# Kernel optimization log

Measured on AMD Instinct MI355X. Metric: run time of the kernel, lower is better.

Reference implementation:

```python
import jax, jax.numpy as jnp
import numpy as np

B, S, D_IN, D_E, H = 512, 100, 300, 150, 2  # batch, patches, patch feat, embed half, heads
L = S + 1  # 101 tokens with class token
EPS = 1e-5


def setup_inputs() -> dict:
    key = jax.random.key(0)
    ks = jax.random.split(key, 12)
    r = lambda k, shp, s=0.02: (jax.random.normal(k, shp, jnp.float32) * s)
    return {
        "x": jax.random.normal(ks[0], (B, S, D_IN), jnp.float32),
        "Wp": r(ks[1], (D_IN, D_E)), "bp": jnp.zeros((D_E,), jnp.float32),
        "pos_table": r(ks[2], (L, D_E), 1.0),
        "class_embed": r(ks[3], (D_E,), 1.0),
        "Wq": r(ks[4], (H, 2 * D_E, 2 * D_E)),
        "Wk": r(ks[5], (H, 2 * D_E, 2 * D_E)),
        "Wv": r(ks[6], (H, 2 * D_E, 2 * D_E)),
        "bn1_g": jnp.ones((L,), jnp.float32), "bn1_b": jnp.zeros((L,), jnp.float32),
        "Wp1": r(ks[7], (900, 300)), "bp1": jnp.zeros((300,), jnp.float32),
        "bn2_g": jnp.ones((L,), jnp.float32), "bn2_b": jnp.zeros((L,), jnp.float32),
        "fc1_W": r(ks[8], (1200, 512)), "fc1_b": jnp.zeros((512,), jnp.float32),
        "fc2_W": r(ks[9], (512, 2)), "fc2_b": jnp.zeros((2,), jnp.float32),
    }


def _batchnorm(x, g, b):
    # torch BatchNorm1d(101) on [B, 101, F]: normalize per channel (dim 1) over (B, F), training-mode batch stats
    mean = jnp.mean(x, axis=(0, 2), keepdims=True)
    var = jnp.var(x, axis=(0, 2), keepdims=True)
    return (x - mean) * jax.lax.rsqrt(var + EPS) * g[None, :, None] + b[None, :, None]


def reference(x, Wp, bp, pos_table, class_embed, Wq, Wk, Wv, bn1_g, bn1_b,
              Wp1, bp1, bn2_g, bn2_b, fc1_W, fc1_b, fc2_W, fc2_b):
    h = jax.nn.relu(x @ Wp + bp)                                   # [B,100,150]
    cls = jnp.concatenate([jnp.broadcast_to(class_embed, (B, D_E)),
                           jnp.broadcast_to(pos_table[0], (B, D_E))], axis=-1)   # [B,300]
    tok = jnp.concatenate([h, jnp.broadcast_to(pos_table[1:], (B, S, D_E))], axis=-1)  # [B,100,300]
    z = jnp.concatenate([cls[:, None, :], tok], axis=1)            # [B,101,300]
    skip1 = jax.lax.stop_gradient(z)                               # x.clone().detach()

    # multi-head self-attention (per-head Q/K/V, no 1/sqrt(d) scaling, matching source)
    Q = jnp.einsum('bsd,hde->hbse', z, Wq)                         # [H,B,101,300]
    K = jnp.einsum('bsd,hde->hbse', z, Wk)
    V = jnp.einsum('bsd,hde->hbse', z, Wv)
    attn = jax.nn.softmax(jnp.einsum('hbse,hbte->hbst', Q, K), axis=-1)  # [H,B,101,101]
    o = jnp.einsum('hbst,hbte->hbse', attn, V)                     # [H,B,101,300]
    msa = jnp.transpose(o, (1, 2, 0, 3)).reshape(B, L, H * 2 * D_E)  # concat heads -> [B,101,600]

    y = _batchnorm(msa, bn1_g, bn1_b)
    y = jnp.concatenate([y, skip1], axis=-1)                       # [B,101,900]
    skip2 = jax.lax.stop_gradient(y)
    y = jax.nn.relu(y @ Wp1 + bp1)                                 # [B,101,300]
    y = _batchnorm(y, bn2_g, bn2_b)
    y = jnp.concatenate([y, skip2], axis=-1)                       # [B,101,1200]
    out = (y[:, 0, :] @ fc1_W + fc1_b) @ fc2_W + fc2_b             # [B,2]
    return out
```

## Files before the change

kernel.cpp:

```cpp
#include <hip/hip_runtime.h>
#include <hip/hip_fp16.h>
#include <math.h>

#define BB 512
#define SS 100
#define DE 150
#define DM 300
#define LL 101
#define NH 2

typedef _Float16 f16x8 __attribute__((ext_vector_type(8)));
typedef float f32x4 __attribute__((ext_vector_type(4)));

#define WS_CLS    0
#define WS_QK     320
#define WS_S0     960
#define WS_CPOS   964
#define WS_CVEC   1200
#define WS_COLSUM 1536
#define WS_CST0   1856
#define WS_STATS  1860
#define WS_G      2176
#define WS_P3     5248
#define WS_PART1  14336
#define WS_PART2  15360
#define WS_MSA    16384
#define WS_Y1     (WS_MSA + 512*600)
#define WS_WPF    477184
#define WS_WVF    502784
#define WS_ZB16   605184
#define WS_Q0P    769024

__global__ void kC1(const float* __restrict__ pos, const float* __restrict__ cle,
                    const float* __restrict__ Wq, const float* __restrict__ Wp1,
                    const float* __restrict__ Wp, const float* __restrict__ Wv,
                    const float* __restrict__ f1W, const float* __restrict__ f2W,
                    const float* __restrict__ f1b, const float* __restrict__ f2b,
                    float* __restrict__ ws) {
  __shared__ float cls[DM];
  int b = blockIdx.x, tid = threadIdx.x;
  if (b < 35) {
    for (int i = tid; i < DM; i += 256) cls[i] = (i < DE) ? cle[i] : pos[i - DE];
    __syncthreads();
  }
  if (b < 20) {
    int p = b >> 1, h = b & 1;
    const float* wqh = Wq + h * DM * DM;
    int d0 = p * 30;
    for (int e = tid; e < DM; e += 256) {
      float acc = 0.f;
#pragma unroll
      for (int d = 0; d < 30; ++d) acc += cls[d0 + d] * wqh[(d0 + d) * DM + e];
      ws[WS_Q0P + p * 600 + h * 300 + e] = acc;
    }
  } else if (b < 35) {
    int kb = b - 20;
    for (int n = tid; n < DM; n += 256) {
      float cs = 0.f, cv = 0.f;
      for (int k = kb * 60; k < kb * 60 + 60; ++k) {
        float w = Wp1[k * 300 + n];
        if (k < 600) cs += w; else cv += cls[k - 600] * w;
      }
      ws[WS_P3 + kb * 600 + n] = cs;
      ws[WS_P3 + kb * 600 + 300 + n] = cv;
    }
  } else if (b == 35) {
    for (int i = tid; i < DM; i += 256)
      ws[WS_CLS + i] = (i < DE) ? cle[i] : pos[i - DE];
  } else if (b < 111) {
    int wave = tid >> 6, lane = tid & 63;
    int kbase = (b - 36) * 16 + wave * 4;
#pragma unroll
    for (int j = 0; j < 4; ++j) {
      int k = kbase + j;
      const float* r = f1W + k * 512;
      float a0 = 0.f, a1 = 0.f;
      for (int m = lane; m < 512; m += 64) {
        float a = r[m];
        float2 f2 = *(const float2*)&f2W[m * 2];
        a0 += a * f2.x; a1 += a * f2.y;
      }
      for (int o = 32; o; o >>= 1) { a0 += __shfl_xor(a0, o); a1 += __shfl_xor(a1, o); }
      if (!lane) { ws[WS_G + k * 2] = a0; ws[WS_G + k * 2 + 1] = a1; }
    }
  } else if (b == 111) {
    int wave = tid >> 6, lane = tid & 63;
    if (wave < 2) {
      float acc = 0.f;
      for (int m = lane; m < 512; m += 64) acc += f1b[m] * f2W[m * 2 + wave];
      for (int o = 32; o; o >>= 1) acc += __shfl_xor(acc, o);
      if (!lane) ws[WS_CST0 + wave] = f2b[wave] + acc;
    }
  } else if (b < 137) {
    int idx = (b - 112) * 256 + tid;
    int kq = idx / 160, n = idx % 160;
    f16x8 pk;
#pragma unroll
    for (int j = 0; j < 8; ++j) {
      int k = kq * 8 + j;
      float v = (k < DM && n < DE) ? Wp[k * DE + n] : 0.f;
      pk[j] = (_Float16)v;
    }
    *(f16x8*)((char*)ws + (size_t)WS_WPF * 4 + (size_t)idx * 16) = pk;
  } else {
    int idx = (b - 137) * 256 + tid;
    int h = idx / 12800, rem = idx % 12800;
    int kq = rem / 320, n = rem % 320;
    f16x8 pk;
#pragma unroll
    for (int j = 0; j < 8; ++j) {
      int k = kq * 8 + j;
      float v = (k < DM && n < DM) ? Wv[h * DM * DM + k * DM + n] : 0.f;
      pk[j] = (_Float16)v;
    }
    *(f16x8*)((char*)ws + (size_t)WS_WVF * 4 + (size_t)idx * 16) = pk;
  }
}

__global__ void kC2(const float* __restrict__ Wk, float* __restrict__ ws) {
  __shared__ float q0s[NH * DM];
  int tid = threadIdx.x;
  for (int i = tid; i < NH * DM; i += 256) {
    float s = 0.f;
#pragma unroll
    for (int p = 0; p < 10; ++p) s += ws[WS_Q0P + p * 600 + i];
    q0s[i] = s;
  }
  __syncthreads();
  int wave = tid >> 6, lane = tid & 63;
  int idx = blockIdx.x * 4 + wave;
  int h = idx / DM, d = idx % DM;
  const float* w = Wk + h * DM * DM + d * DM;
  const float* q = q0s + h * DM;
  float acc = 0.f;
  for (int e = lane; e < DM; e += 64) acc += w[e] * q[e];
  for (int o = 32; o; o >>= 1) acc += __shfl_xor(acc, o);
  if (!lane) ws[WS_QK + idx] = acc;
}

__global__ void kC3(const float* __restrict__ pos, const float* __restrict__ bp1,
                    float* __restrict__ ws) {
  int b = blockIdx.x, tid = threadIdx.x;
  int wave = tid >> 6, lane = tid & 63;
  if (b < 50) {
    int idx = b * 4 + wave;
    int tt = idx >> 1, h = idx & 1;
    const float* pr = pos + (tt + 1) * DE;
    const float* qk = ws + WS_QK + h * DM + DE;
    float acc = 0.f;
    for (int j = lane; j < DE; j += 64) acc += pr[j] * qk[j];
    for (int o = 32; o; o >>= 1) acc += __shfl_xor(acc, o);
    if (!lane) ws[WS_CPOS + idx] = acc;
  } else if (b == 50) {
    if (wave < NH) {
      float acc = 0.f;
      for (int d = lane; d < DM; d += 64) acc += ws[WS_CLS + d] * ws[WS_QK + wave * DM + d];
      for (int o = 32; o; o >>= 1) acc += __shfl_xor(acc, o);
      if (!lane) ws[WS_S0 + wave] = acc;
    }
  } else {
    for (int n = tid; n < DM; n += 256) {
      float cs = 0.f, cv = bp1[n];
      for (int p = 0; p < 15; ++p) {
        cs += ws[WS_P3 + p * 600 + n];
        cv += ws[WS_P3 + p * 600 + 300 + n];
      }
      ws[WS_COLSUM + n] = cs;
      ws[WS_CVEC + n] = cv;
    }
  }
}

__launch_bounds__(512, 4)
__global__ void kA(const float* __restrict__ x, const float* __restrict__ bp,
                   const float* __restrict__ pos, float* __restrict__ ws) {
  __shared__ __align__(16) char smem[41600];
  __half (*hb)[DE + 2] = (__half(*)[DE + 2])smem;
  _Float16* wpt0 = (_Float16*)(smem);
  _Float16* xs0  = (_Float16*)(smem + 10240);
  _Float16* wpt1 = (_Float16*)(smem + 18240);
  _Float16* xs1  = (_Float16*)(smem + 28480);
  float* aux = (float*)(smem + 36480);

  int b = blockIdx.x, tid = threadIdx.x;
  int w = tid >> 6, lane = tid & 63;
  int l16 = lane & 15, lg = lane >> 4;
  int wm = w >> 2, wn = w & 3;
  int nnt = (wn < 3) ? 3 : 1;
  int nt0 = (wn < 3) ? wn * 3 : 9;

  const float* xb = x + b * (SS * DM);
  const char* wpf = (const char*)ws + (size_t)WS_WPF * 4;
  int rowl[4];
#pragma unroll
  for (int mt = 0; mt < 4; ++mt) {
    int r = wm * 64 + mt * 16 + l16;
    rowl[mt] = (r < SS) ? r : (SS - 1);
  }

  f32x4 acc[4][3];
#pragma unroll
  for (int mt = 0; mt < 4; ++mt)
#pragma unroll
    for (int nti = 0; nti < 3; ++nti) acc[mt][nti] = (f32x4){0.f, 0.f, 0.f, 0.f};

  float xr[4][2];
  float4 wa, wb2;

#define XLOAD(S)                                                               \
  { int kc_ = (S) * 32;                                                        \
    _Pragma("unroll")                                                          \
    for (int i_ = 0; i_ < 4; ++i_) {                                           \
      int t_ = tid + 512 * i_;                                                 \
      if (t_ < 1600) {                                                         \
        int r_ = t_ >> 4, c_ = t_ & 15, k_ = kc_ + 2 * c_;                     \
        if (k_ + 1 < DM) {                                                     \
          float2 v_ = *(const float2*)(xb + r_ * DM + k_);                     \
          xr[i_][0] = v_.x; xr[i_][1] = v_.y;                                  \
        } else {                                                               \
          xr[i_][0] = (k_ < DM) ? xb[r_ * DM + k_] : 0.f;                      \
          xr[i_][1] = 0.f;                                                     \
        } } } }

#define XWRITE(XP)                                                             \
  { _Pragma("unroll")                                                          \
    for (int i_ = 0; i_ < 4; ++i_) {                                           \
      int t_ = tid + 512 * i_;                                                 \
      if (t_ < 1600) {                                                         \
        int r_ = t_ >> 4, c_ = t_ & 15;                                        \
        *(__half2*)((char*)(XP) + r_ * 80 + c_ * 4) =                          \
            __floats2half2_rn(xr[i_][0], xr[i_][1]);                           \
      } } }

#define WLOAD(S)                                                               \
  { const char* s_ = wpf + (size_t)(S) * 10240;                                \
    wa = *(const float4*)(s_ + tid * 16);                                      \
    if (tid < 128) wb2 = *(const float4*)(s_ + (tid + 512) * 16); }

#define WWRITE(WP)                                                             \
  { *(float4*)((char*)(WP) + tid * 16) = wa;                                   \
    if (tid < 128) *(float4*)((char*)(WP) + (tid + 512) * 16) = wb2; }

  XLOAD(0); WLOAD(0);
  XWRITE(xs0); WWRITE(wpt0);
  __syncthreads();

  for (int s = 0; s < 10; ++s) {
    _Float16* wc = (s & 1) ? wpt1 : wpt0;
    _Float16* xc = (s & 1) ? xs1 : xs0;
    _Float16* wnx = (s & 1) ? wpt0 : wpt1;
    _Float16* xnx = (s & 1) ? xs0 : xs1;
    if (s < 9) { WLOAD(s + 1); XLOAD(s + 1); }
    f16x8 Bf[3];
#pragma unroll
    for (int nti = 0; nti < 3; ++nti)
      if (nti < nnt)
        Bf[nti] = *(const f16x8*)(wc + ((lg * 160 + (nt0 + nti) * 16 + l16) * 8));
#pragma unroll
    for (int mt = 0; mt < 4; ++mt) {
      f16x8 Af = *(const f16x8*)(xc + rowl[mt] * 40 + lg * 8);
#pragma unroll
      for (int nti = 0; nti < 3; ++nti)
        if (nti < nnt)
          acc[mt][nti] = __builtin_amdgcn_mfma_f32_16x16x32_f16(Af, Bf[nti], acc[mt][nti], 0, 0, 0);
    }
    if (s < 9) { WWRITE(wnx); XWRITE(xnx); }
    __syncthreads();
  }

#pragma unroll
  for (int nti = 0; nti < 3; ++nti) {
    if (nti < nnt) {
      int col = (nt0 + nti) * 16 + l16;
      float bpv = (col < DE) ? bp[col] : 0.f;
#pragma unroll
      for (int mt = 0; mt < 4; ++mt) {
        int rbase = wm * 64 + mt * 16 + lg * 4;
        f32x4 v = acc[mt][nti];
#pragma unroll
        for (int reg = 0; reg < 4; ++reg) {
          int row = rbase + reg;
          if (row < SS && col < DE) {
            float hv = v[reg] + bpv;
            hb[row][col] = __float2half(hv > 0.f ? hv : 0.f);
          }
        }
      }
    }
  }
  for (int i = tid; i < DM; i += 512) {
    aux[i] = ws[WS_QK + (i / DE) * DM + (i % DE)];
    aux[DM + i] = ws[WS_CLS + i];
  }
  __syncthreads();

  if (tid < NH * SS) {
    int hh = tid / SS, tt = tid % SS;
    const __half2* hr = (const __half2*)&hb[tt][0];
    const float* qr = &aux[hh * DE];
    float s = 0.f;
    for (int j2 = 0; j2 < DE / 2; ++j2) {
      float2 hv = __half22float2(hr[j2]);
      float2 qv = *(const float2*)&qr[2 * j2];
      s += hv.x * qv.x + hv.y * qv.y;
    }
    aux[600 + hh * LL + tt + 1] = s + ws[WS_CPOS + tt * NH + hh];
  } else if (tid < NH * SS + NH) {
    int hh = tid - NH * SS;
    aux[600 + hh * LL] = ws[WS_S0 + hh];
  }
  __syncthreads();

  if (w < NH) {
    float v0 = aux[600 + w * LL + lane];
    float v1 = (lane + 64 < LL) ? aux[600 + w * LL + lane + 64] : -1e30f;
    float m = fmaxf(v0, v1);
    for (int o = 32; o; o >>= 1) m = fmaxf(m, __shfl_xor(m, o));
    float e0 = expf(v0 - m);
    float e1 = (lane + 64 < LL) ? expf(v1 - m) : 0.f;
    float s = e0 + e1;
    for (int o = 32; o; o >>= 1) s += __shfl_xor(s, o);
    float inv = 1.f / s;
    aux[802 + w * LL + lane] = e0 * inv;
    if (lane + 64 < LL) aux[802 + w * LL + lane + 64] = e1 * inv;
  }
  __syncthreads();

  __half* zb16 = (__half*)((char*)ws + (size_t)WS_ZB16 * 4);
  for (int o = tid; o < NH * DM; o += 512) {
    int hh = o / DM, d = o % DM;
    const float* p = &aux[802 + hh * LL];
    float acc2 = p[0] * aux[DM + d];
    if (d < DE) {
      for (int t = 1; t <= SS; ++t) acc2 += p[t] * __half2float(hb[t - 1][d]);
    } else {
      int dd = d - DE;
      for (int t = 1; t <= SS; ++t) acc2 += p[t] * pos[t * DE + dd];
    }
    zb16[((size_t)hh * 512 + b) * 320 + d] = __float2half(acc2);
  }
  if (tid < 40) {
    int hh = tid / 20, dd = 300 + tid % 20;
    zb16[((size_t)hh * 512 + b) * 320 + dd] = __float2half(0.f);
  }
}

__launch_bounds__(512, 4)
__global__ void kV(float* __restrict__ ws) {
  __shared__ float shp[2][8];
  int blk = blockIdx.x;
  int mtile = blk >> 2, nb = (blk >> 1) & 1, h = blk & 1;
  int tid = threadIdx.x;
  int w = tid >> 6, lane = tid & 63;
  int l16 = lane & 15, lg = lane >> 4;
  int wm = w >> 2, wn = w & 3;
  int nnt = (wn < 3) ? 3 : 1;
  int nt0 = (wn < 3) ? wn * 3 : 9;
  int mbase = mtile * 128;

  const __half* zb16 = (const __half*)((const char*)ws + (size_t)WS_ZB16 * 4) + (size_t)h * 512 * 320;
  const __half* wvf  = (const __half*)((const char*)ws + (size_t)WS_WVF * 4) + (size_t)h * 40 * 320 * 8;

  int brow[4];
#pragma unroll
  for (int mt = 0; mt < 4; ++mt) brow[mt] = mbase + wm * 64 + mt * 16 + l16;

  f32x4 acc[4][3];
#pragma unroll
  for (int mt = 0; mt < 4; ++mt)
#pragma unroll
    for (int nti = 0; nti < 3; ++nti) acc[mt][nti] = (f32x4){0.f, 0.f, 0.f, 0.f};

  for (int s = 0; s < 10; ++s) {
    f16x8 Bf[3];
#pragma unroll
    for (int nti = 0; nti < 3; ++nti)
      if (nti < nnt) {
        int n = nb * 160 + (nt0 + nti) * 16 + l16;
        Bf[nti] = *(const f16x8*)&wvf[((size_t)(s * 4 + lg) * 320 + n) * 8];
      }
#pragma unroll
    for (int mt = 0; mt < 4; ++mt) {
      f16x8 Af = *(const f16x8*)&zb16[(size_t)brow[mt] * 320 + s * 32 + lg * 8];
#pragma unroll
      for (int nti = 0; nti < 3; ++nti)
        if (nti < nnt)
          acc[mt][nti] = __builtin_amdgcn_mfma_f32_16x16x32_f16(Af, Bf[nti], acc[mt][nti], 0, 0, 0);
    }
  }

  float s_ = 0.f, ss_ = 0.f;
#pragma unroll
  for (int nti = 0; nti < 3; ++nti) {
    if (nti < nnt) {
      int col = nb * 160 + (nt0 + nti) * 16 + l16;
      if (col < DM) {
#pragma unroll
        for (int mt = 0; mt < 4; ++mt) {
          int rbase = mbase + wm * 64 + mt * 16 + lg * 4;
          f32x4 v = acc[mt][nti];
#pragma unroll
          for (int reg = 0; reg < 4; ++reg) {
            int row = rbase + reg;
            float val = v[reg];
            ws[WS_MSA + row * 600 + h * DM + col] = val;
            s_ += val; ss_ += val * val;
          }
        }
      }
    }
  }
  for (int o = 32; o; o >>= 1) { s_ += __shfl_xor(s_, o); ss_ += __shfl_xor(ss_, o); }
  if (!lane) { shp[0][w] = s_; shp[1][w] = ss_; }
  __syncthreads();
  if (!tid) {
    float S = 0.f, SS2 = 0.f;
    for (int i = 0; i < 8; ++i) { S += shp[0][i]; SS2 += shp[1][i]; }
    ws[WS_PART1 + blk * 2] = S;
    ws[WS_PART1 + blk * 2 + 1] = SS2;
  }
}

__launch_bounds__(512)
__global__ void k5(const float* __restrict__ Wp1, const float* __restrict__ g1,
                   const float* __restrict__ b1, float* __restrict__ ws) {
  __shared__ float ab[2][600];
  __shared__ float part[2][2][300];
  __shared__ float sh[2][8];
  __shared__ float s_a1, s_b1;
  int b0 = blockIdx.x * 2, tid = threadIdx.x;
  int wv = tid >> 6, ln = tid & 63;
  for (int i = tid; i < 1200; i += 512) ab[i / 600][i % 600] = ws[WS_MSA + b0 * 600 + i];
  {
    float s = 0.f, ss = 0.f;
    if (tid < 16) { s = ws[WS_PART1 + tid * 2]; ss = ws[WS_PART1 + tid * 2 + 1]; }
    for (int o = 32; o; o >>= 1) { s += __shfl_xor(s, o); ss += __shfl_xor(ss, o); }
    if (!ln) { sh[0][wv] = s; sh[1][wv] = ss; }
  }
  __syncthreads();
  if (!tid) {
    float S = 0.f, SS2 = 0.f;
    for (int i = 0; i < 8; ++i) { S += sh[0][i]; SS2 += sh[1][i]; }
    float n = (float)(BB * 600);
    float mean = S / n, var = SS2 / n - mean * mean;
    float a = (1.f / sqrtf(var + 1e-5f)) * g1[0];
    s_a1 = a; s_b1 = b1[0] - a * mean;
    if (blockIdx.x == 0) { ws[WS_STATS + 0] = a; ws[WS_STATS + 1] = s_b1; }
  }
  __syncthreads();
  int g = tid >> 8, t = tid & 255;
  int kbeg = g * 300, kend = kbeg + 300;
  for (int n = t; n < 300; n += 256) {
    float a0 = 0.f, a1v = 0.f;
    for (int k = kbeg; k < kend; ++k) {
      float wq = Wp1[k * 300 + n];
      a0 += ab[0][k] * wq;
      a1v += ab[1][k] * wq;
    }
    part[g][0][n] = a0;
    part[g][1][n] = a1v;
  }
  __syncthreads();
  float a1 = s_a1, beta1 = s_b1;
  float s2 = 0.f, ss2 = 0.f;
  for (int n = tid; n < 300; n += 512) {
    float c = beta1 * ws[WS_COLSUM + n] + ws[WS_CVEC + n];
    float v0 = a1 * (part[0][0][n] + part[1][0][n]) + c;
    float v1 = a1 * (part[0][1][n] + part[1][1][n]) + c;
    v0 = v0 > 0.f ? v0 : 0.f;
    v1 = v1 > 0.f ? v1 : 0.f;
    ws[WS_Y1 + b0 * 300 + n] = v0;
    ws[WS_Y1 + (b0 + 1) * 300 + n] = v1;
    s2 += v0 + v1; ss2 += v0 * v0 + v1 * v1;
  }
  for (int o = 32; o; o >>= 1) { s2 += __shfl_xor(s2, o); ss2 += __shfl_xor(ss2, o); }
  if (!ln) { sh[0][wv] = s2; sh[1][wv] = ss2; }
  __syncthreads();
  if (!tid) {
    float S = 0.f, SS2 = 0.f;
    for (int i = 0; i < 8; ++i) { S += sh[0][i]; SS2 += sh[1][i]; }
    ws[WS_PART2 + blockIdx.x * 2] = S;
    ws[WS_PART2 + blockIdx.x * 2 + 1] = SS2;
  }
}

__launch_bounds__(256)
__global__ void k7(const float* __restrict__ g2, const float* __restrict__ b2,
                   float* __restrict__ out, const float* __restrict__ ws) {
  __shared__ float Gs[2400];
  __shared__ float sh[2][4];
  __shared__ float cc[4];
  int tid = threadIdx.x, wv = tid >> 6, ln = tid & 63;
  for (int i = tid; i < 2400; i += 256) Gs[i] = ws[WS_G + i];
  {
    float s = ws[WS_PART2 + tid * 2], ss = ws[WS_PART2 + tid * 2 + 1];
    for (int o = 32; o; o >>= 1) { s += __shfl_xor(s, o); ss += __shfl_xor(ss, o); }
    if (!ln) { sh[0][wv] = s; sh[1][wv] = ss; }
  }
  __syncthreads();
  if (!tid) {
    float S = 0.f, SS2 = 0.f;
    for (int i = 0; i < 4; ++i) { S += sh[0][i]; SS2 += sh[1][i]; }
    float n = (float)(BB * 300);
    float mean = S / n, var = SS2 / n - mean * mean;
    float a = (1.f / sqrtf(var + 1e-5f)) * g2[0];
    cc[0] = a; cc[1] = b2[0] - a * mean;
  }
  __syncthreads();
  if (tid < 2) {
    int c = tid;
    float sg1 = 0.f, sg2 = 0.f, sg3 = 0.f;
    for (int k = 0; k < 300; ++k) sg1 += Gs[k * 2 + c];
    for (int k = 300; k < 900; ++k) sg2 += Gs[k * 2 + c];
    for (int j = 0; j < 300; ++j) sg3 += ws[WS_CLS + j] * Gs[(900 + j) * 2 + c];
    cc[2 + c] = ws[WS_CST0 + c] + sg3 + cc[1] * sg1 + ws[WS_STATS + 1] * sg2;
  }
  __syncthreads();
  int b = blockIdx.x * 4 + wv;
  float a1 = ws[WS_STATS + 0], a2 = cc[0];
  const float* y1 = ws + WS_Y1 + b * 300;
  const float* ms = ws + WS_MSA + b * 600;
  float o0 = 0.f, o1 = 0.f, p0 = 0.f, p1 = 0.f;
  for (int k = ln; k < 300; k += 64) { float v = y1[k]; o0 += v * Gs[k * 2]; o1 += v * Gs[k * 2 + 1]; }
  for (int j = ln; j < 600; j += 64) { float v = ms[j]; p0 += v * Gs[(300 + j) * 2]; p1 += v * Gs[(300 + j) * 2 + 1]; }
  for (int o = 32; o; o >>= 1) {
    o0 += __shfl_xor(o0, o); o1 += __shfl_xor(o1, o);
    p0 += __shfl_xor(p0, o); p1 += __shfl_xor(p1, o);
  }
  if (!ln) {
    out[b * 2] = a2 * o0 + a1 * p0 + cc[2];
    out[b * 2 + 1] = a2 * o1 + a1 * p1 + cc[3];
  }
}

extern "C" void kernel_launch(void* const* d_in, const int* in_sizes, int n_in,
                              void* d_out, int out_size, void* d_ws, size_t ws_size,
                              hipStream_t stream) {
  const float* x    = (const float*)d_in[0];
  const float* Wp   = (const float*)d_in[1];
  const float* bp   = (const float*)d_in[2];
  const float* pos  = (const float*)d_in[3];
  const float* cle  = (const float*)d_in[4];
  const float* Wq   = (const float*)d_in[5];
  const float* Wk   = (const float*)d_in[6];
  const float* Wv   = (const float*)d_in[7];
  const float* bn1g = (const float*)d_in[8];
  const float* bn1b = (const float*)d_in[9];
  const float* Wp1  = (const float*)d_in[10];
  const float* bp1  = (const float*)d_in[11];
  const float* bn2g = (const float*)d_in[12];
  const float* bn2b = (const float*)d_in[13];
  const float* f1W  = (const float*)d_in[14];
  const float* f1b  = (const float*)d_in[15];
  const float* f2W  = (const float*)d_in[16];
  const float* f2b  = (const float*)d_in[17];
  float* ws = (float*)d_ws;
  float* out = (float*)d_out;

  hipLaunchKernelGGL(kC1, dim3(237), dim3(256), 0, stream, pos, cle, Wq, Wp1, Wp, Wv, f1W, f2W, f1b, f2b, ws);
  hipLaunchKernelGGL(kC2, dim3(150), dim3(256), 0, stream, Wk, ws);
  hipLaunchKernelGGL(kC3, dim3(52), dim3(256), 0, stream, pos, bp1, ws);
  hipLaunchKernelGGL(kA, dim3(512), dim3(512), 0, stream, x, bp, pos, ws);
  hipLaunchKernelGGL(kV, dim3(16), dim3(512), 0, stream, ws);
  hipLaunchKernelGGL(k5, dim3(256), dim3(512), 0, stream, Wp1, bn1g, bn1b, ws);
  hipLaunchKernelGGL(k7, dim3(128), dim3(256), 0, stream, bn2g, bn2b, out, ws);
}
```

Baseline: 117.1 us.

## Convert k5 projection GEMM to fp16 MFMA using packed MSA and Wp1 tiles

kV now also writes an fp16 copy of the MSA output, padded to 608 columns. kC1 gains extra blocks that pack the first 600 rows of Wp1 into fp16 k-octets. k5 changes from a scalar FP32 two-rows-per-block loop (256 blocks) to an MFMA 16x16x32 tiled GEMM over 128-row by 160-column tiles (8 blocks), with the BN-affine, ReLU and partial-stats epilogue fused in. The aim is to replace slow scalar FMA work on the 512x600x300 product with matrix cores, at the cost of fp16 precision loss and only 8 blocks of parallelism.

```diff
diff --git a/kernel.cpp b/kernel.cpp
--- a/kernel.cpp
+++ b/kernel.cpp
@@ -30,6 +30,8 @@
 #define WS_WVF    502784
 #define WS_ZB16   605184
 #define WS_Q0P    769024
+#define WS_MSA16  775040
+#define WS_WP1F   930688
 
 __global__ void kC1(const float* __restrict__ pos, const float* __restrict__ cle,
                     const float* __restrict__ Wq, const float* __restrict__ Wp1,
@@ -102,7 +104,7 @@
       pk[j] = (_Float16)v;
     }
     *(f16x8*)((char*)ws + (size_t)WS_WPF * 4 + (size_t)idx * 16) = pk;
-  } else {
+  } else if (b < 237) {
     int idx = (b - 137) * 256 + tid;
     int h = idx / 12800, rem = idx % 12800;
     int kq = rem / 320, n = rem % 320;
@@ -114,6 +116,17 @@
       pk[j] = (_Float16)v;
     }
     *(f16x8*)((char*)ws + (size_t)WS_WVF * 4 + (size_t)idx * 16) = pk;
+  } else {
+    int idx = (b - 237) * 256 + tid;
+    int kq = idx / 320, n = idx % 320;
+    f16x8 pk;
+#pragma unroll
+    for (int j = 0; j < 8; ++j) {
+      int k = kq * 8 + j;
+      float v = (k < 600 && n < DM) ? Wp1[k * 300 + n] : 0.f;
+      pk[j] = (_Float16)v;
+    }
+    *(f16x8*)((char*)ws + (size_t)WS_WP1F * 4 + (size_t)idx * 16) = pk;
   }
 }
 
@@ -360,6 +373,7 @@
 
   const __half* zb16 = (const __half*)((const char*)ws + (size_t)WS_ZB16 * 4) + (size_t)h * 512 * 320;
   const __half* wvf  = (const __half*)((const char*)ws + (size_t)WS_WVF * 4) + (size_t)h * 40 * 320 * 8;
+  __half* msa16h = (__half*)((char*)ws + (size_t)WS_MSA16 * 4);
 
   int brow[4];
 #pragma unroll
@@ -404,10 +418,17 @@
             int row = rbase + reg;
             float val = v[reg];
             ws[WS_MSA + row * 600 + h * DM + col] = val;
+            msa16h[(size_t)row * 608 + h * DM + col] = __float2half(val);
             s_ += val; ss_ += val * val;
           }
         }
       }
+    }
+  }
+  if (nb == 1 && h == 1) {
+    for (int i = tid; i < 128 * 8; i += 512) {
+      int r = mbase + (i >> 3), c = 600 + (i & 7);
+      msa16h[(size_t)r * 608 + c] = __float2half(0.f);
     }
   }
   for (int o = 32; o; o >>= 1) { s_ += __shfl_xor(s_, o); ss_ += __shfl_xor(ss_, o); }
@@ -421,21 +442,29 @@
   }
 }
 
-__launch_bounds__(512)
-__global__ void k5(const float* __restrict__ Wp1, const float* __restrict__ g1,
-                   const float* __restrict__ b1, float* __restrict__ ws) {
-  __shared__ float ab[2][600];
-  __shared__ float part[2][2][300];
+__launch_bounds__(512, 4)
+__global__ void k5(const float* __restrict__ g1, const float* __restrict__ b1,
+                   float* __restrict__ ws) {
   __shared__ float sh[2][8];
-  __shared__ float s_a1, s_b1;
-  int b0 = blockIdx.x * 2, tid = threadIdx.x;
-  int wv = tid >> 6, ln = tid & 63;
-  for (int i = tid; i < 1200; i += 512) ab[i / 600][i % 600] = ws[WS_MSA + b0 * 600 + i];
+  __shared__ float s_ab[2];
+  int blk = blockIdx.x;
+  int mtile = blk >> 1, nb = blk & 1;
+  int tid = threadIdx.x;
+  int w = tid >> 6, lane = tid & 63;
+  int l16 = lane & 15, lg = lane >> 4;
+  int wm = w >> 2, wn = w & 3;
+  int nnt = (wn < 3) ? 3 : 1;
+  int nt0 = (wn < 3) ? wn * 3 : 9;
+  int mbase = mtile * 128;
+
+  const __half* msa16h = (const __half*)((const char*)ws + (size_t)WS_MSA16 * 4);
+  const __half* wp1f   = (const __half*)((const char*)ws + (size_t)WS_WP1F * 4);
+
   {
     float s = 0.f, ss = 0.f;
     if (tid < 16) { s = ws[WS_PART1 + tid * 2]; ss = ws[WS_PART1 + tid * 2 + 1]; }
     for (int o = 32; o; o >>= 1) { s += __shfl_xor(s, o); ss += __shfl_xor(ss, o); }
-    if (!ln) { sh[0][wv] = s; sh[1][wv] = ss; }
+    if (!lane) { sh[0][w] = s; sh[1][w] = ss; }
   }
   __syncthreads();
   if (!tid) {
@@ -444,43 +473,71 @@
     float n = (float)(BB * 600);
     float mean = S / n, var = SS2 / n - mean * mean;
     float a = (1.f / sqrtf(var + 1e-5f)) * g1[0];
-    s_a1 = a; s_b1 = b1[0] - a * mean;
-    if (blockIdx.x == 0) { ws[WS_STATS + 0] = a; ws[WS_STATS + 1] = s_b1; }
-  }
-  __syncthreads();
-  int g = tid >> 8, t = tid & 255;
-  int kbeg = g * 300, kend = kbeg + 300;
-  for (int n = t; n < 300; n += 256) {
-    float a0 = 0.f, a1v = 0.f;
-    for (int k = kbeg; k < kend; ++k) {
-      float wq = Wp1[k * 300 + n];
-      a0 += ab[0][k] * wq;
-      a1v += ab[1][k] * wq;
-    }
-    part[g][0][n] = a0;
-    part[g][1][n] = a1v;
-  }
-  __syncthreads();
-  float a1 = s_a1, beta1 = s_b1;
+    s_ab[0] = a; s_ab[1] = b1[0] - a * mean;
+    if (blk == 0) { ws[WS_STATS + 0] = a; ws[WS_STATS + 1] = s_ab[1]; }
+  }
+  __syncthreads();
+
+  int brow[4];
+#pragma unroll
+  for (int mt = 0; mt < 4; ++mt) brow[mt] = mbase + wm * 64 + mt * 16 + l16;
+
+  f32x4 acc[4][3];
+#pragma unroll
+  for (int mt = 0; mt < 4; ++mt)
+#pragma unroll
+    for (int nti = 0; nti < 3; ++nti) acc[mt][nti] = (f32x4){0.f, 0.f, 0.f, 0.f};
+
+  for (int s = 0; s < 19; ++s) {
+    f16x8 Bf[3];
+#pragma unroll
+    for (int nti = 0; nti < 3; ++nti)
+      if (nti < nnt) {
+        int n = nb * 160 + (nt0 + nti) * 16 + l16;
+        Bf[nti] = *(const f16x8*)&wp1f[((size_t)(s * 4 + lg) * 320 + n) * 8];
+      }
+#pragma unroll
+    for (int mt = 0; mt < 4; ++mt) {
+      f16x8 Af = *(const f16x8*)&msa16h[(size_t)brow[mt] * 608 + s * 32 + lg * 8];
+#pragma unroll
+      for (int nti = 0; nti < 3; ++nti)
+        if (nti < nnt)
+          acc[mt][nti] = __builtin_amdgcn_mfma_f32_16x16x32_f16(Af, Bf[nti], acc[mt][nti], 0, 0, 0);
+    }
+  }
+
+  float a1 = s_ab[0], beta1 = s_ab[1];
   float s2 = 0.f, ss2 = 0.f;
-  for (int n = tid; n < 300; n += 512) {
-    float c = beta1 * ws[WS_COLSUM + n] + ws[WS_CVEC + n];
-    float v0 = a1 * (part[0][0][n] + part[1][0][n]) + c;
-    float v1 = a1 * (part[0][1][n] + part[1][1][n]) + c;
-    v0 = v0 > 0.f ? v0 : 0.f;
-    v1 = v1 > 0.f ? v1 : 0.f;
-    ws[WS_Y1 + b0 * 300 + n] = v0;
-    ws[WS_Y1 + (b0 + 1) * 300 + n] = v1;
-    s2 += v0 + v1; ss2 += v0 * v0 + v1 * v1;
+#pragma unroll
+  for (int nti = 0; nti < 3; ++nti) {
+    if (nti < nnt) {
+      int col = nb * 160 + (nt0 + nti) * 16 + l16;
+      if (col < DM) {
+        float c = beta1 * ws[WS_COLSUM + col] + ws[WS_CVEC + col];
+#pragma unroll
+        for (int mt = 0; mt < 4; ++mt) {
+          int rbase = mbase + wm * 64 + mt * 16 + lg * 4;
+          f32x4 v = acc[mt][nti];
+#pragma unroll
+          for (int reg = 0; reg < 4; ++reg) {
+            int row = rbase + reg;
+            float val = a1 * v[reg] + c;
+            val = val > 0.f ? val : 0.f;
+            ws[WS_Y1 + row * 300 + col] = val;
+            s2 += val; ss2 += val * val;
+          }
+        }
+      }
+    }
   }
   for (int o = 32; o; o >>= 1) { s2 += __shfl_xor(s2, o); ss2 += __shfl_xor(ss2, o); }
-  if (!ln) { sh[0][wv] = s2; sh[1][wv] = ss2; }
+  if (!lane) { sh[0][w] = s2; sh[1][w] = ss2; }
   __syncthreads();
   if (!tid) {
     float S = 0.f, SS2 = 0.f;
     for (int i = 0; i < 8; ++i) { S += sh[0][i]; SS2 += sh[1][i]; }
-    ws[WS_PART2 + blockIdx.x * 2] = S;
-    ws[WS_PART2 + blockIdx.x * 2 + 1] = SS2;
+    ws[WS_PART2 + blk * 2] = S;
+    ws[WS_PART2 + blk * 2 + 1] = SS2;
   }
 }
 
@@ -493,7 +550,8 @@
   int tid = threadIdx.x, wv = tid >> 6, ln = tid & 63;
   for (int i = tid; i < 2400; i += 256) Gs[i] = ws[WS_G + i];
   {
-    float s = ws[WS_PART2 + tid * 2], ss = ws[WS_PART2 + tid * 2 + 1];
+    float s = 0.f, ss = 0.f;
+    if (tid < 8) { s = ws[WS_PART2 + tid * 2]; ss = ws[WS_PART2 + tid * 2 + 1]; }
     for (int o = 32; o; o >>= 1) { s += __shfl_xor(s, o); ss += __shfl_xor(ss, o); }
     if (!ln) { sh[0][wv] = s; sh[1][wv] = ss; }
   }
@@ -557,11 +615,11 @@
   float* ws = (float*)d_ws;
   float* out = (float*)d_out;
 
-  hipLaunchKernelGGL(kC1, dim3(237), dim3(256), 0, stream, pos, cle, Wq, Wp1, Wp, Wv, f1W, f2W, f1b, f2b, ws);
+  hipLaunchKernelGGL(kC1, dim3(332), dim3(256), 0, stream, pos, cle, Wq, Wp1, Wp, Wv, f1W, f2W, f1b, f2b, ws);
   hipLaunchKernelGGL(kC2, dim3(150), dim3(256), 0, stream, Wk, ws);
   hipLaunchKernelGGL(kC3, dim3(52), dim3(256), 0, stream, pos, bp1, ws);
   hipLaunchKernelGGL(kA, dim3(512), dim3(512), 0, stream, x, bp, pos, ws);
   hipLaunchKernelGGL(kV, dim3(16), dim3(512), 0, stream, ws);
-  hipLaunchKernelGGL(k5, dim3(256), dim3(512), 0, stream, Wp1, bn1g, bn1b, ws);
+  hipLaunchKernelGGL(k5, dim3(8), dim3(512), 0, stream, bn1g, bn1b, ws);
   hipLaunchKernelGGL(k7, dim3(128), dim3(256), 0, stream, bn2g, bn2b, out, ws);
 }
```

New measurement: 125.0 us. 1.07x slower.

## Merge tail kernels into cooperative grid-sync kernel and fold kC3 into kA

Applied to the files above, without the earlier changes.

Removes kC3 by moving the per-token positional score and class-token score into kA, where each block recomputes them from shared memory, and folds the column-sum reduction into an extra block of kC2. The three tail kernels kV, k5 and k7 become one cooperative kernel that uses grid.sync between phases, cutting launch count from seven to four. The aim is to remove kernel-launch gaps and dependency bubbles. In exchange, every kA block does a little redundant work, and the cooperative launch needs all 256 blocks co-resident while only 16 blocks run the GEMM phase.

```diff
diff --git a/kernel.cpp b/kernel.cpp
--- a/kernel.cpp
+++ b/kernel.cpp
@@ -1,6 +1,9 @@
 #include <hip/hip_runtime.h>
 #include <hip/hip_fp16.h>
+#include <hip/hip_cooperative_groups.h>
 #include <math.h>
+
+namespace cg = cooperative_groups;
 
 #define BB 512
 #define SS 100
@@ -14,8 +17,6 @@
 
 #define WS_CLS    0
 #define WS_QK     320
-#define WS_S0     960
-#define WS_CPOS   964
 #define WS_CVEC   1200
 #define WS_COLSUM 1536
 #define WS_CST0   1856
@@ -117,9 +118,22 @@
   }
 }
 
-__global__ void kC2(const float* __restrict__ Wk, float* __restrict__ ws) {
+__global__ void kC2p(const float* __restrict__ Wk, const float* __restrict__ bp1,
+                     float* __restrict__ ws) {
+  int b = blockIdx.x, tid = threadIdx.x;
+  if (b == 150) {
+    for (int n = tid; n < DM; n += 256) {
+      float cs = 0.f, cv = bp1[n];
+      for (int p = 0; p < 15; ++p) {
+        cs += ws[WS_P3 + p * 600 + n];
+        cv += ws[WS_P3 + p * 600 + 300 + n];
+      }
+      ws[WS_COLSUM + n] = cs;
+      ws[WS_CVEC + n] = cv;
+    }
+    return;
+  }
   __shared__ float q0s[NH * DM];
-  int tid = threadIdx.x;
   for (int i = tid; i < NH * DM; i += 256) {
     float s = 0.f;
 #pragma unroll
@@ -128,7 +142,7 @@
   }
   __syncthreads();
   int wave = tid >> 6, lane = tid & 63;
-  int idx = blockIdx.x * 4 + wave;
+  int idx = b * 4 + wave;
   int h = idx / DM, d = idx % DM;
   const float* w = Wk + h * DM * DM + d * DM;
   const float* q = q0s + h * DM;
@@ -138,43 +152,10 @@
   if (!lane) ws[WS_QK + idx] = acc;
 }
 
-__global__ void kC3(const float* __restrict__ pos, const float* __restrict__ bp1,
-                    float* __restrict__ ws) {
-  int b = blockIdx.x, tid = threadIdx.x;
-  int wave = tid >> 6, lane = tid & 63;
-  if (b < 50) {
-    int idx = b * 4 + wave;
-    int tt = idx >> 1, h = idx & 1;
-    const float* pr = pos + (tt + 1) * DE;
-    const float* qk = ws + WS_QK + h * DM + DE;
-    float acc = 0.f;
-    for (int j = lane; j < DE; j += 64) acc += pr[j] * qk[j];
-    for (int o = 32; o; o >>= 1) acc += __shfl_xor(acc, o);
-    if (!lane) ws[WS_CPOS + idx] = acc;
-  } else if (b == 50) {
-    if (wave < NH) {
-      float acc = 0.f;
-      for (int d = lane; d < DM; d += 64) acc += ws[WS_CLS + d] * ws[WS_QK + wave * DM + d];
-      for (int o = 32; o; o >>= 1) acc += __shfl_xor(acc, o);
-      if (!lane) ws[WS_S0 + wave] = acc;
-    }
-  } else {
-    for (int n = tid; n < DM; n += 256) {
-      float cs = 0.f, cv = bp1[n];
-      for (int p = 0; p < 15; ++p) {
-        cs += ws[WS_P3 + p * 600 + n];
-        cv += ws[WS_P3 + p * 600 + 300 + n];
-      }
-      ws[WS_COLSUM + n] = cs;
-      ws[WS_CVEC + n] = cv;
-    }
-  }
-}
-
 __launch_bounds__(512, 4)
 __global__ void kA(const float* __restrict__ x, const float* __restrict__ bp,
                    const float* __restrict__ pos, float* __restrict__ ws) {
-  __shared__ __align__(16) char smem[41600];
+  __shared__ __align__(16) char smem[41696];
   __half (*hb)[DE + 2] = (__half(*)[DE + 2])smem;
   _Float16* wpt0 = (_Float16*)(smem);
   _Float16* xs0  = (_Float16*)(smem + 10240);
@@ -288,32 +269,44 @@
       }
     }
   }
-  for (int i = tid; i < DM; i += 512) {
-    aux[i] = ws[WS_QK + (i / DE) * DM + (i % DE)];
-    aux[DM + i] = ws[WS_CLS + i];
+  for (int i = tid; i < 600; i += 512) aux[i] = ws[WS_QK + i];
+  for (int i = tid; i < DM; i += 512) aux[600 + i] = ws[WS_CLS + i];
+  __syncthreads();
+
+  if (tid < 400) {
+    int o = tid >> 1, half = tid & 1;
+    int tt = o >> 1, hh = o & 1;
+    const float* pr = pos + (tt + 1) * DE;
+    const float* qk2 = &aux[hh * 300 + DE];
+    float s = 0.f;
+    for (int j = half; j < DE; j += 2) s += pr[j] * qk2[j];
+    s += __shfl_xor(s, 1);
+    if (!half) aux[900 + hh * LL + tt + 1] = s;
+  } else if (tid == 400 || tid == 401) {
+    int hh = tid - 400;
+    float s = 0.f;
+    for (int d = 0; d < DM; ++d) s += aux[600 + d] * aux[hh * 300 + d];
+    aux[900 + hh * LL] = s;
   }
   __syncthreads();
 
   if (tid < NH * SS) {
     int hh = tid / SS, tt = tid % SS;
     const __half2* hr = (const __half2*)&hb[tt][0];
-    const float* qr = &aux[hh * DE];
+    const float* qr = &aux[hh * 300];
     float s = 0.f;
     for (int j2 = 0; j2 < DE / 2; ++j2) {
       float2 hv = __half22float2(hr[j2]);
       float2 qv = *(const float2*)&qr[2 * j2];
       s += hv.x * qv.x + hv.y * qv.y;
     }
-    aux[600 + hh * LL + tt + 1] = s + ws[WS_CPOS + tt * NH + hh];
-  } else if (tid < NH * SS + NH) {
-    int hh = tid - NH * SS;
-    aux[600 + hh * LL] = ws[WS_S0 + hh];
+    aux[900 + hh * LL + tt + 1] += s;
   }
   __syncthreads();
 
   if (w < NH) {
-    float v0 = aux[600 + w * LL + lane];
-    float v1 = (lane + 64 < LL) ? aux[600 + w * LL + lane + 64] : -1e30f;
+    float v0 = aux[900 + w * LL + lane];
+    float v1 = (lane + 64 < LL) ? aux[900 + w * LL + lane + 64] : -1e30f;
     float m = fmaxf(v0, v1);
     for (int o = 32; o; o >>= 1) m = fmaxf(m, __shfl_xor(m, o));
     float e0 = expf(v0 - m);
@@ -321,16 +314,16 @@
     float s = e0 + e1;
     for (int o = 32; o; o >>= 1) s += __shfl_xor(s, o);
     float inv = 1.f / s;
-    aux[802 + w * LL + lane] = e0 * inv;
-    if (lane + 64 < LL) aux[802 + w * LL + lane + 64] = e1 * inv;
+    aux[1102 + w * LL + lane] = e0 * inv;
+    if (lane + 64 < LL) aux[1102 + w * LL + lane + 64] = e1 * inv;
   }
   __syncthreads();
 
   __half* zb16 = (__half*)((char*)ws + (size_t)WS_ZB16 * 4);
   for (int o = tid; o < NH * DM; o += 512) {
     int hh = o / DM, d = o % DM;
-    const float* p = &aux[802 + hh * LL];
-    float acc2 = p[0] * aux[DM + d];
+    const float* p = &aux[1102 + hh * LL];
+    float acc2 = p[0] * aux[600 + d];
     if (d < DE) {
       for (int t = 1; t <= SS; ++t) acc2 += p[t] * __half2float(hb[t - 1][d]);
     } else {
@@ -345,191 +338,188 @@
   }
 }
 
-__launch_bounds__(512, 4)
-__global__ void kV(float* __restrict__ ws) {
-  __shared__ float shp[2][8];
-  int blk = blockIdx.x;
-  int mtile = blk >> 2, nb = (blk >> 1) & 1, h = blk & 1;
-  int tid = threadIdx.x;
+__launch_bounds__(512)
+__global__ void kTail(const float* __restrict__ Wp1, const float* __restrict__ g1,
+                      const float* __restrict__ b1, const float* __restrict__ g2,
+                      const float* __restrict__ b2, float* __restrict__ out,
+                      float* __restrict__ ws) {
+  cg::grid_group grid = cg::this_grid();
+  __shared__ __align__(16) float sm[2424];
+  int blk = blockIdx.x, tid = threadIdx.x;
   int w = tid >> 6, lane = tid & 63;
-  int l16 = lane & 15, lg = lane >> 4;
-  int wm = w >> 2, wn = w & 3;
-  int nnt = (wn < 3) ? 3 : 1;
-  int nt0 = (wn < 3) ? wn * 3 : 9;
-  int mbase = mtile * 128;
-
-  const __half* zb16 = (const __half*)((const char*)ws + (size_t)WS_ZB16 * 4) + (size_t)h * 512 * 320;
-  const __half* wvf  = (const __half*)((const char*)ws + (size_t)WS_WVF * 4) + (size_t)h * 40 * 320 * 8;
-
-  int brow[4];
-#pragma unroll
-  for (int mt = 0; mt < 4; ++mt) brow[mt] = mbase + wm * 64 + mt * 16 + l16;
-
-  f32x4 acc[4][3];
-#pragma unroll
-  for (int mt = 0; mt < 4; ++mt)
-#pragma unroll
-    for (int nti = 0; nti < 3; ++nti) acc[mt][nti] = (f32x4){0.f, 0.f, 0.f, 0.f};
-
-  for (int s = 0; s < 10; ++s) {
-    f16x8 Bf[3];
-#pragma unroll
-    for (int nti = 0; nti < 3; ++nti)
+
+  if (blk < 16) {
+    int mtile = blk >> 2, nb = (blk >> 1) & 1, h = blk & 1;
+    int l16 = lane & 15, lg = lane >> 4;
+    int wm = w >> 2, wn = w & 3;
+    int nnt = (wn < 3) ? 3 : 1;
+    int nt0 = (wn < 3) ? wn * 3 : 9;
+    int mbase = mtile * 128;
+    const __half* zb16 = (const __half*)((const char*)ws + (size_t)WS_ZB16 * 4) + (size_t)h * 512 * 320;
+    const __half* wvf  = (const __half*)((const char*)ws + (size_t)WS_WVF * 4) + (size_t)h * 40 * 320 * 8;
+    int brow[4];
+#pragma unroll
+    for (int mt = 0; mt < 4; ++mt) brow[mt] = mbase + wm * 64 + mt * 16 + l16;
+    f32x4 acc[4][3];
+#pragma unroll
+    for (int mt = 0; mt < 4; ++mt)
+#pragma unroll
+      for (int nti = 0; nti < 3; ++nti) acc[mt][nti] = (f32x4){0.f, 0.f, 0.f, 0.f};
+    for (int s = 0; s < 10; ++s) {
+      f16x8 Bf[3];
+#pragma unroll
+      for (int nti = 0; nti < 3; ++nti)
+        if (nti < nnt) {
+          int n = nb * 160 + (nt0 + nti) * 16 + l16;
+          Bf[nti] = *(const f16x8*)&wvf[((size_t)(s * 4 + lg) * 320 + n) * 8];
+        }
+#pragma unroll
+      for (int mt = 0; mt < 4; ++mt) {
+        f16x8 Af = *(const f16x8*)&zb16[(size_t)brow[mt] * 320 + s * 32 + lg * 8];
+#pragma unroll
+        for (int nti = 0; nti < 3; ++nti)
+          if (nti < nnt)
+            acc[mt][nti] = __builtin_amdgcn_mfma_f32_16x16x32_f16(Af, Bf[nti], acc[mt][nti], 0, 0, 0);
+      }
+    }
+    float s_ = 0.f, ss_ = 0.f;
+#pragma unroll
+    for (int nti = 0; nti < 3; ++nti) {
       if (nti < nnt) {
-        int n = nb * 160 + (nt0 + nti) * 16 + l16;
-        Bf[nti] = *(const f16x8*)&wvf[((size_t)(s * 4 + lg) * 320 + n) * 8];
-      }
-#pragma unroll
-    for (int mt = 0; mt < 4; ++mt) {
-      f16x8 Af = *(const f16x8*)&zb16[(size_t)brow[mt] * 320 + s * 32 + lg * 8];
-#pragma unroll
-      for (int nti = 0; nti < 3; ++nti)
-        if (nti < nnt)
-          acc[mt][nti] = __builtin_amdgcn_mfma_f32_16x16x32_f16(Af, Bf[nti], acc[mt][nti], 0, 0, 0);
-    }
-  }
-
-  float s_ = 0.f, ss_ = 0.f;
-#pragma unroll
-  for (int nti = 0; nti < 3; ++nti) {
-    if (nti < nnt) {
-      int col = nb * 160 + (nt0 + nti) * 16 + l16;
-      if (col < DM) {
-#pragma unroll
-        for (int mt = 0; mt < 4; ++mt) {
-          int rbase = mbase + wm * 64 + mt * 16 + lg * 4;
-          f32x4 v = acc[mt][nti];
-#pragma unroll
-          for (int reg = 0; reg < 4; ++reg) {
-            int row = rbase + reg;
-            float val = v[reg];
-            ws[WS_MSA + row * 600 + h * DM + col] = val;
-            s_ += val; ss_ += val * val;
+        int col = nb * 160 + (nt0 + nti) * 16 + l16;
+        if (col < DM) {
+#pragma unroll
+          for (int mt = 0; mt < 4; ++mt) {
+            int rbase = mbase + wm * 64 + mt * 16 + lg * 4;
+            f32x4 v = acc[mt][nti];
+#pragma unroll
+            for (int reg = 0; reg < 4; ++reg) {
+              float val = v[reg];
+              ws[WS_MSA + (rbase + reg) * 600 + h * DM + col] = val;
+              s_ += val; ss_ += val * val;
+            }
           }
         }
       }
     }
-  }
-  for (int o = 32; o; o >>= 1) { s_ += __shfl_xor(s_, o); ss_ += __shfl_xor(ss_, o); }
-  if (!lane) { shp[0][w] = s_; shp[1][w] = ss_; }
-  __syncthreads();
-  if (!tid) {
-    float S = 0.f, SS2 = 0.f;
-    for (int i = 0; i < 8; ++i) { S += shp[0][i]; SS2 += shp[1][i]; }
-    ws[WS_PART1 + blk * 2] = S;
-    ws[WS_PART1 + blk * 2 + 1] = SS2;
-  }
-}
-
-__launch_bounds__(512)
-__global__ void k5(const float* __restrict__ Wp1, const float* __restrict__ g1,
-                   const float* __restrict__ b1, float* __restrict__ ws) {
-  __shared__ float ab[2][600];
-  __shared__ float part[2][2][300];
-  __shared__ float sh[2][8];
-  __shared__ float s_a1, s_b1;
-  int b0 = blockIdx.x * 2, tid = threadIdx.x;
-  int wv = tid >> 6, ln = tid & 63;
-  for (int i = tid; i < 1200; i += 512) ab[i / 600][i % 600] = ws[WS_MSA + b0 * 600 + i];
+    for (int o = 32; o; o >>= 1) { s_ += __shfl_xor(s_, o); ss_ += __shfl_xor(ss_, o); }
+    if (!lane) { sm[2400 + w] = s_; sm[2408 + w] = ss_; }
+    __syncthreads();
+    if (!tid) {
+      float S = 0.f, SS2 = 0.f;
+      for (int i = 0; i < 8; ++i) { S += sm[2400 + i]; SS2 += sm[2408 + i]; }
+      ws[WS_PART1 + blk * 2] = S;
+      ws[WS_PART1 + blk * 2 + 1] = SS2;
+    }
+  }
+  grid.sync();
+
   {
-    float s = 0.f, ss = 0.f;
-    if (tid < 16) { s = ws[WS_PART1 + tid * 2]; ss = ws[WS_PART1 + tid * 2 + 1]; }
-    for (int o = 32; o; o >>= 1) { s += __shfl_xor(s, o); ss += __shfl_xor(ss, o); }
-    if (!ln) { sh[0][wv] = s; sh[1][wv] = ss; }
-  }
-  __syncthreads();
-  if (!tid) {
-    float S = 0.f, SS2 = 0.f;
-    for (int i = 0; i < 8; ++i) { S += sh[0][i]; SS2 += sh[1][i]; }
-    float n = (float)(BB * 600);
-    float mean = S / n, var = SS2 / n - mean * mean;
-    float a = (1.f / sqrtf(var + 1e-5f)) * g1[0];
-    s_a1 = a; s_b1 = b1[0] - a * mean;
-    if (blockIdx.x == 0) { ws[WS_STATS + 0] = a; ws[WS_STATS + 1] = s_b1; }
-  }
-  __syncthreads();
-  int g = tid >> 8, t = tid & 255;
-  int kbeg = g * 300, kend = kbeg + 300;
-  for (int n = t; n < 300; n += 256) {
-    float a0 = 0.f, a1v = 0.f;
-    for (int k = kbeg; k < kend; ++k) {
-      float wq = Wp1[k * 300 + n];
-      a0 += ab[0][k] * wq;
-      a1v += ab[1][k] * wq;
-    }
-    part[g][0][n] = a0;
-    part[g][1][n] = a1v;
-  }
-  __syncthreads();
-  float a1 = s_a1, beta1 = s_b1;
-  float s2 = 0.f, ss2 = 0.f;
-  for (int n = tid; n < 300; n += 512) {
-    float c = beta1 * ws[WS_COLSUM + n] + ws[WS_CVEC + n];
-    float v0 = a1 * (part[0][0][n] + part[1][0][n]) + c;
-    float v1 = a1 * (part[0][1][n] + part[1][1][n]) + c;
-    v0 = v0 > 0.f ? v0 : 0.f;
-    v1 = v1 > 0.f ? v1 : 0.f;
-    ws[WS_Y1 + b0 * 300 + n] = v0;
-    ws[WS_Y1 + (b0 + 1) * 300 + n] = v1;
-    s2 += v0 + v1; ss2 += v0 * v0 + v1 * v1;
-  }
-  for (int o = 32; o; o >>= 1) { s2 += __shfl_xor(s2, o); ss2 += __shfl_xor(ss2, o); }
-  if (!ln) { sh[0][wv] = s2; sh[1][wv] = ss2; }
-  __syncthreads();
-  if (!tid) {
-    float S = 0.f, SS2 = 0.f;
-    for (int i = 0; i < 8; ++i) { S += sh[0][i]; SS2 += sh[1][i]; }
-    ws[WS_PART2 + blockIdx.x * 2] = S;
-    ws[WS_PART2 + blockIdx.x * 2 + 1] = SS2;
-  }
-}
-
-__launch_bounds__(256)
-__global__ void k7(const float* __restrict__ g2, const float* __restrict__ b2,
-                   float* __restrict__ out, const float* __restrict__ ws) {
-  __shared__ float Gs[2400];
-  __shared__ float sh[2][4];
-  __shared__ float cc[4];
-  int tid = threadIdx.x, wv = tid >> 6, ln = tid & 63;
-  for (int i = tid; i < 2400; i += 256) Gs[i] = ws[WS_G + i];
-  {
-    float s = ws[WS_PART2 + tid * 2], ss = ws[WS_PART2 + tid * 2 + 1];
-    for (int o = 32; o; o >>= 1) { s += __shfl_xor(s, o); ss += __shfl_xor(ss, o); }
-    if (!ln) { sh[0][wv] = s; sh[1][wv] = ss; }
-  }
-  __syncthreads();
-  if (!tid) {
-    float S = 0.f, SS2 = 0.f;
-    for (int i = 0; i < 4; ++i) { S += sh[0][i]; SS2 += sh[1][i]; }
-    float n = (float)(BB * 300);
-    float mean = S / n, var = SS2 / n - mean * mean;
-    float a = (1.f / sqrtf(var + 1e-5f)) * g2[0];
-    cc[0] = a; cc[1] = b2[0] - a * mean;
-  }
-  __syncthreads();
-  if (tid < 2) {
-    int c = tid;
-    float sg1 = 0.f, sg2 = 0.f, sg3 = 0.f;
-    for (int k = 0; k < 300; ++k) sg1 += Gs[k * 2 + c];
-    for (int k = 300; k < 900; ++k) sg2 += Gs[k * 2 + c];
-    for (int j = 0; j < 300; ++j) sg3 += ws[WS_CLS + j] * Gs[(900 + j) * 2 + c];
-    cc[2 + c] = ws[WS_CST0 + c] + sg3 + cc[1] * sg1 + ws[WS_STATS + 1] * sg2;
-  }
-  __syncthreads();
-  int b = blockIdx.x * 4 + wv;
-  float a1 = ws[WS_STATS + 0], a2 = cc[0];
-  const float* y1 = ws + WS_Y1 + b * 300;
-  const float* ms = ws + WS_MSA + b * 600;
-  float o0 = 0.f, o1 = 0.f, p0 = 0.f, p1 = 0.f;
-  for (int k = ln; k < 300; k += 64) { float v = y1[k]; o0 += v * Gs[k * 2]; o1 += v * Gs[k * 2 + 1]; }
-  for (int j = ln; j < 600; j += 64) { float v = ms[j]; p0 += v * Gs[(300 + j) * 2]; p1 += v * Gs[(300 + j) * 2 + 1]; }
-  for (int o = 32; o; o >>= 1) {
-    o0 += __shfl_xor(o0, o); o1 += __shfl_xor(o1, o);
-    p0 += __shfl_xor(p0, o); p1 += __shfl_xor(p1, o);
-  }
-  if (!ln) {
-    out[b * 2] = a2 * o0 + a1 * p0 + cc[2];
-    out[b * 2 + 1] = a2 * o1 + a1 * p1 + cc[3];
+    float* ab   = sm;
+    float* part = sm + 1200;
+    float* shr  = sm + 2400;
+    float* s_ab = sm + 2416;
+    int b0 = blk * 2;
+    for (int i = tid; i < 1200; i += 512) ab[i] = ws[WS_MSA + b0 * 600 + i];
+    {
+      float s = 0.f, ss = 0.f;
+      if (tid < 16) { s = ws[WS_PART1 + tid * 2]; ss = ws[WS_PART1 + tid * 2 + 1]; }
+      for (int o = 32; o; o >>= 1) { s += __shfl_xor(s, o); ss += __shfl_xor(ss, o); }
+      if (!lane) { shr[w] = s; shr[8 + w] = ss; }
+    }
+    __syncthreads();
+    if (!tid) {
+      float S = 0.f, SS2 = 0.f;
+      for (int i = 0; i < 8; ++i) { S += shr[i]; SS2 += shr[8 + i]; }
+      float n = (float)(BB * 600);
+      float mean = S / n, var = SS2 / n - mean * mean;
+      float a = (1.f / sqrtf(var + 1e-5f)) * g1[0];
+      s_ab[0] = a; s_ab[1] = b1[0] - a * mean;
+      if (blk == 0) { ws[WS_STATS + 0] = a; ws[WS_STATS + 1] = s_ab[1]; }
+    }
+    __syncthreads();
+    int g = tid >> 8, t = tid & 255;
+    int kbeg = g * 300, kend = kbeg + 300;
+    for (int n = t; n < 300; n += 256) {
+      float a0 = 0.f, a1v = 0.f;
+      for (int k = kbeg; k < kend; ++k) {
+        float wq = Wp1[k * 300 + n];
+        a0 += ab[k] * wq;
+        a1v += ab[600 + k] * wq;
+      }
+      part[g * 600 + n] = a0;
+      part[g * 600 + 300 + n] = a1v;
+    }
+    __syncthreads();
+    float a1 = s_ab[0], beta1 = s_ab[1];
+    float s2 = 0.f, ss2 = 0.f;
+    for (int n = tid; n < 300; n += 512) {
+      float c = beta1 * ws[WS_COLSUM + n] + ws[WS_CVEC + n];
+      float v0 = a1 * (part[n] + part[600 + n]) + c;
+      float v1 = a1 * (part[300 + n] + part[900 + n]) + c;
+      v0 = v0 > 0.f ? v0 : 0.f;
+      v1 = v1 > 0.f ? v1 : 0.f;
+      ws[WS_Y1 + b0 * 300 + n] = v0;
+      ws[WS_Y1 + (b0 + 1) * 300 + n] = v1;
+      s2 += v0 + v1; ss2 += v0 * v0 + v1 * v1;
+    }
+    for (int o = 32; o; o >>= 1) { s2 += __shfl_xor(s2, o); ss2 += __shfl_xor(ss2, o); }
+    if (!lane) { shr[w] = s2; shr[8 + w] = ss2; }
+    __syncthreads();
+    if (!tid) {
+      float S = 0.f, SS2 = 0.f;
+      for (int i = 0; i < 8; ++i) { S += shr[i]; SS2 += shr[8 + i]; }
+      ws[WS_PART2 + blk * 2] = S;
+      ws[WS_PART2 + blk * 2 + 1] = SS2;
+    }
+  }
+  grid.sync();
+
+  if (blk < 64) {
+    float* Gs  = sm;
+    float* shr = sm + 2400;
+    float* cc  = sm + 2416;
+    for (int i = tid; i < 2400; i += 512) Gs[i] = ws[WS_G + i];
+    {
+      float s = 0.f, ss = 0.f;
+      if (tid < 256) { s = ws[WS_PART2 + tid * 2]; ss = ws[WS_PART2 + tid * 2 + 1]; }
+      for (int o = 32; o; o >>= 1) { s += __shfl_xor(s, o); ss += __shfl_xor(ss, o); }
+      if (!lane) { shr[w] = s; shr[8 + w] = ss; }
+    }
+    __syncthreads();
+    if (!tid) {
+      float S = 0.f, SS2 = 0.f;
+      for (int i = 0; i < 8; ++i) { S += shr[i]; SS2 += shr[8 + i]; }
+      float n = (float)(BB * 300);
+      float mean = S / n, var = SS2 / n - mean * mean;
+      float a = (1.f / sqrtf(var + 1e-5f)) * g2[0];
+      cc[0] = a; cc[1] = b2[0] - a * mean;
+    }
+    __syncthreads();
+    if (tid < 2) {
+      int c = tid;
+      float sg1 = 0.f, sg2 = 0.f, sg3 = 0.f;
+      for (int k = 0; k < 300; ++k) sg1 += Gs[k * 2 + c];
+      for (int k = 300; k < 900; ++k) sg2 += Gs[k * 2 + c];
+      for (int j = 0; j < 300; ++j) sg3 += ws[WS_CLS + j] * Gs[(900 + j) * 2 + c];
+      cc[2 + c] = ws[WS_CST0 + c] + sg3 + cc[1] * sg1 + ws[WS_STATS + 1] * sg2;
+    }
+    __syncthreads();
+    int b = blk * 8 + w;
+    float a1 = ws[WS_STATS + 0], a2 = cc[0];
+    const float* y1 = ws + WS_Y1 + b * 300;
+    const float* ms = ws + WS_MSA + b * 600;
+    float o0 = 0.f, o1 = 0.f, p0 = 0.f, p1 = 0.f;
+    for (int k = lane; k < 300; k += 64) { float v = y1[k]; o0 += v * Gs[k * 2]; o1 += v * Gs[k * 2 + 1]; }
+    for (int j = lane; j < 600; j += 64) { float v = ms[j]; p0 += v * Gs[(300 + j) * 2]; p1 += v * Gs[(300 + j) * 2 + 1]; }
+    for (int o = 32; o; o >>= 1) {
+      o0 += __shfl_xor(o0, o); o1 += __shfl_xor(o1, o);
+      p0 += __shfl_xor(p0, o); p1 += __shfl_xor(p1, o);
+    }
+    if (!lane) {
+      out[b * 2] = a2 * o0 + a1 * p0 + cc[2];
+      out[b * 2 + 1] = a2 * o1 + a1 * p1 + cc[3];
+    }
   }
 }
 
@@ -558,10 +548,9 @@
   float* out = (float*)d_out;
 
   hipLaunchKernelGGL(kC1, dim3(237), dim3(256), 0, stream, pos, cle, Wq, Wp1, Wp, Wv, f1W, f2W, f1b, f2b, ws);
-  hipLaunchKernelGGL(kC2, dim3(150), dim3(256), 0, stream, Wk, ws);
-  hipLaunchKernelGGL(kC3, dim3(52), dim3(256), 0, stream, pos, bp1, ws);
+  hipLaunchKernelGGL(kC2p, dim3(151), dim3(256), 0, stream, Wk, bp1, ws);
   hipLaunchKernelGGL(kA, dim3(512), dim3(512), 0, stream, x, bp, pos, ws);
-  hipLaunchKernelGGL(kV, dim3(16), dim3(512), 0, stream, ws);
-  hipLaunchKernelGGL(k5, dim3(256), dim3(512), 0, stream, Wp1, bn1g, bn1b, ws);
-  hipLaunchKernelGGL(k7, dim3(128), dim3(256), 0, stream, bn2g, bn2b, out, ws);
+  void* kt_args[] = {(void*)&Wp1, (void*)&bn1g, (void*)&bn1b, (void*)&bn2g,
+                     (void*)&bn2b, (void*)&out, (void*)&ws};
+  hipLaunchCooperativeKernel((void*)kTail, dim3(256), dim3(512), kt_args, 0, stream);
 }
```

Measured after the change: 188.0 us. 60.5% more time.
